# Optimization experiments

Hardware: AMD Instinct MI355X
Metric: run time of the kernel (lower is better)

Reference implementation:

```python
import jax, jax.numpy as jnp
import numpy as np

L = 104          # atom feature / hidden dim (self.length)
NUM_CLASSES = 500
D, N, P = 256, 1024, 8  # DAGs, nodes per DAG (topo-ordered), max predecessors


def setup_inputs() -> dict:
    key = jax.random.key(0)
    ks = jax.random.split(key, 8)
    atom_features = jax.random.normal(ks[0], (D, N, L), dtype=jnp.float32)

    # Padded predecessor lists; pred_idx[d, n, p] < n guarantees topological order 0..N-1.
    rng = np.random.default_rng(0)
    base = np.floor(rng.random((D, N, P)) * np.maximum(np.arange(N), 1)[None, :, None]).astype(np.int32)
    keep = rng.random((D, N, P)) < 0.6
    keep[:, :, 0] = True                      # every non-root node has >=1 predecessor
    pred_idx = np.where(keep, base, -1)
    pred_idx[:, 0, :] = -1                    # node 0 is the root (no predecessors)
    pred_idx = jnp.asarray(pred_idx, dtype=jnp.int32)

    s1 = float(1.0 / np.sqrt(L))
    s2 = float(1.0 / np.sqrt(2 * L))
    W_single = jax.random.uniform(ks[1], (L, L), minval=-s1, maxval=s1)
    b_single = jax.random.uniform(ks[2], (L,), minval=-s1, maxval=s1)
    W_merge = jax.random.uniform(ks[3], (L, 2 * L), minval=-s2, maxval=s2)
    b_merge = jax.random.uniform(ks[4], (L,), minval=-s2, maxval=s2)
    attn_w = jax.random.uniform(ks[5], (L,))   # torch.rand(length)
    dag_w = jax.random.uniform(ks[6], (L,))
    W_final = jax.random.uniform(ks[7], (NUM_CLASSES, L), minval=-s1, maxval=s1)
    b_final = jnp.zeros((NUM_CLASSES,), jnp.float32)
    return {
        "atom_features": atom_features, "pred_idx": pred_idx,
        "W_single": W_single, "b_single": b_single,
        "W_merge": W_merge, "b_merge": b_merge,
        "attn_w": attn_w, "dag_w": dag_w,
        "W_final": W_final, "b_final": b_final,
    }


def _forward(atom_features, pred_idx, W_single, b_single, W_merge, b_merge,
             attn_w, dag_w, W_final, b_final):
    n_nodes = atom_features.shape[1]

    def per_dag(feats, preds):  # feats [N, L], preds [N, P]
        def step(outputs, n):
            feat = feats[n]                                   # [L]
            p = preds[n]                                      # [P]
            valid = p >= 0                                    # [P]
            po = outputs[jnp.clip(p, 0, n_nodes - 1)]         # [P, L] gathered predecessor outputs
            # softmax over the predecessor (stacking) dim, weighted by attention_weight
            logits = jnp.where(valid[:, None], attn_w * po, -1e30)
            agg = jnp.sum(jax.nn.softmax(logits, axis=0) * po * valid[:, None].astype(po.dtype), axis=0)  # [L]
            merged = jax.nn.relu(W_merge @ jnp.concatenate([agg, feat]) + b_merge)
            root = jax.nn.relu(W_single @ feat + b_single)
            out = jnp.where(jnp.any(valid), merged, root)     # [L]
            return outputs.at[n].set(out), None
        outputs, _ = jax.lax.scan(step, jnp.zeros_like(feats), jnp.arange(n_nodes))
        return outputs[-1]                                    # output of last (sink) node

    last = jax.vmap(per_dag)(atom_features, pred_idx)         # [D, L]
    w = jax.nn.softmax(dag_w * last, axis=0)                  # softmax over DAG dim
    pooled = jnp.sum(w * last, axis=0)                        # [L]
    return pooled @ W_final.T + b_final                       # [NUM_CLASSES]


def reference(atom_features, pred_idx, W_single, b_single, W_merge, b_merge,
              attn_w, dag_w, W_final, b_final):
    return _forward(atom_features, pred_idx, W_single, b_single, W_merge, b_merge,
                    attn_w, dag_w, W_final, b_final)
```

## Files before the change

kernel.cpp:

```cpp
#include <hip/hip_runtime.h>

#define DN  256
#define NN  1024
#define PP  8
#define LL  104
#define CLS 500
#define BT  512
#define TMAX 64
#define KP  232
#define NG  26

typedef __attribute__((ext_vector_type(8))) short short8;
typedef __attribute__((ext_vector_type(4))) short short4v;
typedef __attribute__((ext_vector_type(4))) float f32x4;

#define MFMA(a, b, c) __builtin_amdgcn_mfma_f32_16x16x32_bf16((a), (b), (c), 0, 0, 0)

__device__ __forceinline__ void split_bf16(float x, unsigned short& h, unsigned short& l) {
    unsigned u = __float_as_uint(x);
    h = (unsigned short)(u >> 16);
    float hf = __uint_as_float(u & 0xFFFF0000u);
    l = (unsigned short)(__float_as_uint(x - hf) >> 16);
}

__global__ __launch_bounds__(BT, 2) void dag_level_kernel(
    const float* __restrict__ atom,
    const int*   __restrict__ pred,
    const float* __restrict__ W_single,
    const float* __restrict__ b_single,
    const float* __restrict__ W_merge,
    const float* __restrict__ b_merge,
    const float* __restrict__ attn_w,
    float* __restrict__ out_all,
    float* __restrict__ last_buf)
{
    __shared__ __align__(16) unsigned short x_hi[TMAX][KP];
    __shared__ __align__(16) unsigned short x_lo[TMAX][KP];
    __shared__ int   lvl[NN];
    __shared__ int   cnt[NN];
    __shared__ unsigned short order[NN];
    __shared__ __align__(16) float s_attn[LL];
    __shared__ float s_bm[LL];
    __shared__ int   csum[64];
    __shared__ int   s_flag, s_maxlvl;

    const int d    = blockIdx.x;
    const int tid  = threadIdx.x;
    const int wid  = tid >> 6;
    const int lane = tid & 63;
    const int p    = wid & 3;

    const float* atom_d = atom + (size_t)d * NN * LL;
    const int*   pred_d = pred + (size_t)d * NN * PP;
    float*       out_d  = out_all + (size_t)d * NN * LL;

    short8 wh[2][7], wl[2][7];
    #pragma unroll
    for (int h = 0; h < 2; ++h) {
        const int r = (2*p + h)*16 + (lane & 15);
        #pragma unroll
        for (int kt = 0; kt < 7; ++kt) {
            const int k0 = kt*32 + (lane >> 4)*8;
            short8 hh, lo8;
            #pragma unroll
            for (int j = 0; j < 8; ++j) {
                float v = (r < LL && (k0 + j) < 2*LL) ? W_merge[r*2*LL + k0 + j] : 0.f;
                unsigned short a, b;
                split_bf16(v, a, b);
                hh[j] = (short)a; lo8[j] = (short)b;
            }
            wh[h][kt] = hh; wl[h][kt] = lo8;
        }
    }

    for (int idx = tid; idx < TMAX * (KP - 2*LL); idx += BT) {
        int rr = idx / (KP - 2*LL), cc = 2*LL + (idx - rr*(KP - 2*LL));
        x_hi[rr][cc] = 0; x_lo[rr][cc] = 0;
    }
    if (tid < LL) { s_attn[tid] = attn_w[tid]; s_bm[tid] = b_merge[tid]; }
    if (tid == 0) { s_flag = 0; s_maxlvl = 0; }

    int mypA[PP], mypB[PP];
    {
        const int4* p4 = (const int4*)(pred_d + tid * PP);
        int4 a = p4[0], b = p4[1];
        mypA[0]=a.x; mypA[1]=a.y; mypA[2]=a.z; mypA[3]=a.w;
        mypA[4]=b.x; mypA[5]=b.y; mypA[6]=b.z; mypA[7]=b.w;
        const int4* q4 = (const int4*)(pred_d + (tid + BT) * PP);
        int4 c = q4[0], e = q4[1];
        mypB[0]=c.x; mypB[1]=c.y; mypB[2]=c.z; mypB[3]=c.w;
        mypB[4]=e.x; mypB[5]=e.y; mypB[6]=e.z; mypB[7]=e.w;
    }
    lvl[tid] = 0; lvl[tid + BT] = 0;
    __syncthreads();
    for (int it = 1; it <= NN; ++it) {
        int mxA = -1, mxB = -1;
        #pragma unroll
        for (int q = 0; q < PP; ++q) {
            if (mypA[q] >= 0) mxA = max(mxA, lvl[mypA[q]]);
            if (mypB[q] >= 0) mxB = max(mxB, lvl[mypB[q]]);
        }
        bool ch = false;
        if (mxA + 1 != lvl[tid])      { lvl[tid]      = mxA + 1; ch = true; }
        if (mxB + 1 != lvl[tid + BT]) { lvl[tid + BT] = mxB + 1; ch = true; }
        if (ch) s_flag = it;
        __syncthreads();
        int f = s_flag;
        __syncthreads();
        if (f != it) break;
    }
    atomicMax(&s_maxlvl, max(lvl[tid], lvl[tid + BT]));

    cnt[tid] = 0; cnt[tid + BT] = 0;
    __syncthreads();
    atomicAdd(&cnt[lvl[tid]], 1);
    atomicAdd(&cnt[lvl[tid + BT]], 1);
    __syncthreads();
    if (tid < 64) { int s = 0; for (int i = 0; i < 16; ++i) s += cnt[tid*16 + i]; csum[tid] = s; }
    __syncthreads();
    if (tid == 0) { int run = 0; for (int t = 0; t < 64; ++t) { int c = csum[t]; csum[t] = run; run += c; } }
    __syncthreads();
    if (tid < 64) {
        int run = csum[tid];
        for (int i = 0; i < 16; ++i) { int c = cnt[tid*16 + i]; cnt[tid*16 + i] = run; run += c; }
    }
    __syncthreads();
    {
        int pos = atomicAdd(&cnt[lvl[tid]], 1);      order[pos] = (unsigned short)tid;
        pos     = atomicAdd(&cnt[lvl[tid + BT]], 1); order[pos] = (unsigned short)(tid + BT);
    }
    __syncthreads();

    {
        int nroots = cnt[0];
        for (int task = tid; task < nroots * LL; task += BT) {
            int ni = task / LL, r = task - ni * LL;
            int n = order[ni];
            float acc = b_single[r];
            const float* feat = atom_d + n * LL;
            const float* wr = W_single + r * LL;
            #pragma unroll 8
            for (int l = 0; l < LL; ++l) acc = fmaf(wr[l], feat[l], acc);
            float v = fmaxf(acc, 0.f);
            out_d[n * LL + r] = v;
            if (n == NN - 1) last_buf[d * LL + r] = v;
        }
    }
    __syncthreads();

    const int maxlvl = s_maxlvl;
    for (int L = 1; L <= maxlvl; ++L) {
        const int s = cnt[L - 1], e = cnt[L];
        for (int t0 = s; t0 < e; t0 += TMAX) {
            const int tc = min(TMAX, e - t0);

            const int ntask = tc * NG;
            for (int task = tid; task < ntask; task += BT) {
                int ni = task / NG;
                int lg = task - ni * NG;
                int n  = order[t0 + ni];
                const int4* pp4 = (const int4*)(pred_d + n * PP);
                int4 pa = pp4[0], pb = pp4[1];
                int pi[PP] = {pa.x, pa.y, pa.z, pa.w, pb.x, pb.y, pb.z, pb.w};
                float4 aw = *(const float4*)&s_attn[lg*4];
                float4 ft = *(const float4*)&atom_d[n*LL + lg*4];
                float awv[4] = {aw.x, aw.y, aw.z, aw.w};
                float ftv[4] = {ft.x, ft.y, ft.z, ft.w};
                float po[PP][4];
                #pragma unroll
                for (int q = 0; q < PP; ++q) {
                    if (pi[q] >= 0) {
                        float4 t = *(const float4*)&out_d[pi[q]*LL + lg*4];
                        po[q][0] = t.x; po[q][1] = t.y; po[q][2] = t.z; po[q][3] = t.w;
                    } else {
                        po[q][0] = po[q][1] = po[q][2] = po[q][3] = 0.f;
                    }
                }
                unsigned short oh[8], ol[8];
                #pragma unroll
                for (int f = 0; f < 4; ++f) {
                    float m = -1e30f;
                    #pragma unroll
                    for (int q = 0; q < PP; ++q)
                        if (pi[q] >= 0) m = fmaxf(m, awv[f] * po[q][f]);
                    float den = 0.f, num = 0.f;
                    #pragma unroll
                    for (int q = 0; q < PP; ++q) {
                        if (pi[q] >= 0) {
                            float e2 = __expf(fmaf(awv[f], po[q][f], -m));
                            den += e2;
                            num = fmaf(e2, po[q][f], num);
                        }
                    }
                    float agg = __fdividef(num, den);
                    split_bf16(agg,    oh[f],     ol[f]);
                    split_bf16(ftv[f], oh[4 + f], ol[4 + f]);
                }
                short4v h0 = {(short)oh[0], (short)oh[1], (short)oh[2], (short)oh[3]};
                short4v l0 = {(short)ol[0], (short)ol[1], (short)ol[2], (short)ol[3]};
                short4v h1 = {(short)oh[4], (short)oh[5], (short)oh[6], (short)oh[7]};
                short4v l1 = {(short)ol[4], (short)ol[5], (short)ol[6], (short)ol[7]};
                *(short4v*)&x_hi[ni][lg*4]      = h0;
                *(short4v*)&x_lo[ni][lg*4]      = l0;
                *(short4v*)&x_hi[ni][LL + lg*4] = h1;
                *(short4v*)&x_lo[ni][LL + lg*4] = l1;
            }
            __syncthreads();

            const int mts = (tc + 15) >> 4;
            const int njobs = mts * 4;
            for (int job = wid; job < njobs; job += 8) {
                const int mt = job >> 2;
                const int row_a = mt*16 + (lane & 15);
                const int kg = (lane >> 4) * 8;
                f32x4 acc0 = {0.f,0.f,0.f,0.f}, acc1 = {0.f,0.f,0.f,0.f};
                #pragma unroll
                for (int kt = 0; kt < 7; ++kt) {
                    const int k0 = kt*32 + kg;
                    short8 ah = *(const short8*)&x_hi[row_a][k0];
                    short8 al = *(const short8*)&x_lo[row_a][k0];
                    acc0 = MFMA(ah, wh[0][kt], acc0);
                    acc0 = MFMA(ah, wl[0][kt], acc0);
                    acc0 = MFMA(al, wh[0][kt], acc0);
                    if (p < 3) {
                        acc1 = MFMA(ah, wh[1][kt], acc1);
                        acc1 = MFMA(ah, wl[1][kt], acc1);
                        acc1 = MFMA(al, wh[1][kt], acc1);
                    }
                }
                const int r0 = p*32 + (lane & 15);
                #pragma unroll
                for (int j = 0; j < 4; ++j) {
                    int ni = mt*16 + (lane >> 4)*4 + j;
                    if (ni < tc) {
                        int n = order[t0 + ni];
                        if (r0 < LL) {
                            float v = fmaxf(acc0[j] + s_bm[r0], 0.f);
                            out_d[n*LL + r0] = v;
                            if (n == NN - 1) last_buf[d*LL + r0] = v;
                        }
                        if (p < 3) {
                            const int r1 = r0 + 16;
                            float v = fmaxf(acc1[j] + s_bm[r1], 0.f);
                            out_d[n*LL + r1] = v;
                            if (n == NN - 1) last_buf[d*LL + r1] = v;
                        }
                    }
                }
            }
            __syncthreads();
        }
    }
}

__global__ __launch_bounds__(256) void final_pool_kernel(
    const float* __restrict__ last_buf,
    const float* __restrict__ dag_w,
    const float* __restrict__ W_final,
    const float* __restrict__ b_final,
    float* __restrict__ out)
{
    __shared__ float s_pooled[LL];
    const int tid = threadIdx.x;

    if (tid < LL) {
        float dw = dag_w[tid];
        float m = -1e30f;
        #pragma unroll 8
        for (int dd = 0; dd < DN; ++dd)
            m = fmaxf(m, dw * last_buf[dd * LL + tid]);
        float den = 0.f, num = 0.f;
        #pragma unroll 8
        for (int dd = 0; dd < DN; ++dd) {
            float v = last_buf[dd * LL + tid];
            float e = __expf(dw * v - m);
            den += e;
            num = fmaf(e, v, num);
        }
        s_pooled[tid] = num / den;
    }
    __syncthreads();

    for (int c = tid; c < CLS; c += 256) {
        float acc = b_final[c];
        const float* wr = W_final + c * LL;
        #pragma unroll 8
        for (int l = 0; l < LL; ++l) acc = fmaf(wr[l], s_pooled[l], acc);
        out[c] = acc;
    }
}

extern "C" void kernel_launch(void* const* d_in, const int* in_sizes, int n_in,
                              void* d_out, int out_size, void* d_ws, size_t ws_size,
                              hipStream_t stream) {
    const float* atom     = (const float*)d_in[0];
    const int*   pred     = (const int*)  d_in[1];
    const float* W_single = (const float*)d_in[2];
    const float* b_single = (const float*)d_in[3];
    const float* W_merge  = (const float*)d_in[4];
    const float* b_merge  = (const float*)d_in[5];
    const float* attn_w   = (const float*)d_in[6];
    const float* dag_w    = (const float*)d_in[7];
    const float* W_final  = (const float*)d_in[8];
    const float* b_final  = (const float*)d_in[9];
    float* out = (float*)d_out;

    float* out_all  = (float*)d_ws;
    float* last_buf = out_all + (size_t)DN * NN * LL;

    dag_level_kernel<<<DN, BT, 0, stream>>>(atom, pred, W_single, b_single,
                                            W_merge, b_merge, attn_w,
                                            out_all, last_buf);
    final_pool_kernel<<<1, 256, 0, stream>>>(last_buf, dag_w, W_final, b_final, out);
}
```

Measured before the change: 396.1 us.

## Prefetch next tile's predecessor gathers across the MFMA phase and split accumulators

```diff
diff --git a/kernel.cpp b/kernel.cpp
--- a/kernel.cpp
+++ b/kernel.cpp
@@ -80,8 +80,8 @@
     if (tid < LL) { s_attn[tid] = attn_w[tid]; s_bm[tid] = b_merge[tid]; }
     if (tid == 0) { s_flag = 0; s_maxlvl = 0; }
 
-    int mypA[PP], mypB[PP];
     {
+        int mypA[PP], mypB[PP];
         const int4* p4 = (const int4*)(pred_d + tid * PP);
         int4 a = p4[0], b = p4[1];
         mypA[0]=a.x; mypA[1]=a.y; mypA[2]=a.z; mypA[3]=a.w;
@@ -90,26 +90,26 @@
         int4 c = q4[0], e = q4[1];
         mypB[0]=c.x; mypB[1]=c.y; mypB[2]=c.z; mypB[3]=c.w;
         mypB[4]=e.x; mypB[5]=e.y; mypB[6]=e.z; mypB[7]=e.w;
-    }
-    lvl[tid] = 0; lvl[tid + BT] = 0;
-    __syncthreads();
-    for (int it = 1; it <= NN; ++it) {
-        int mxA = -1, mxB = -1;
-        #pragma unroll
-        for (int q = 0; q < PP; ++q) {
-            if (mypA[q] >= 0) mxA = max(mxA, lvl[mypA[q]]);
-            if (mypB[q] >= 0) mxB = max(mxB, lvl[mypB[q]]);
+        lvl[tid] = 0; lvl[tid + BT] = 0;
+        __syncthreads();
+        for (int it = 1; it <= NN; ++it) {
+            int mxA = -1, mxB = -1;
+            #pragma unroll
+            for (int q = 0; q < PP; ++q) {
+                if (mypA[q] >= 0) mxA = max(mxA, lvl[mypA[q]]);
+                if (mypB[q] >= 0) mxB = max(mxB, lvl[mypB[q]]);
+            }
+            bool ch = false;
+            if (mxA + 1 != lvl[tid])      { lvl[tid]      = mxA + 1; ch = true; }
+            if (mxB + 1 != lvl[tid + BT]) { lvl[tid + BT] = mxB + 1; ch = true; }
+            if (ch) s_flag = it;
+            __syncthreads();
+            int f = s_flag;
+            __syncthreads();
+            if (f != it) break;
         }
-        bool ch = false;
-        if (mxA + 1 != lvl[tid])      { lvl[tid]      = mxA + 1; ch = true; }
-        if (mxB + 1 != lvl[tid + BT]) { lvl[tid + BT] = mxB + 1; ch = true; }
-        if (ch) s_flag = it;
-        __syncthreads();
-        int f = s_flag;
-        __syncthreads();
-        if (f != it) break;
-    }
-    atomicMax(&s_maxlvl, max(lvl[tid], lvl[tid + BT]));
+        atomicMax(&s_maxlvl, max(lvl[tid], lvl[tid + BT]));
+    }
 
     cnt[tid] = 0; cnt[tid + BT] = 0;
     __syncthreads();
@@ -149,63 +149,147 @@
     __syncthreads();
 
     const int maxlvl = s_maxlvl;
+
+    int    pf_pi[PP];
+    float  pf_po[PP][4];
+    float4 pf_ft = {0.f, 0.f, 0.f, 0.f};
+    int    pf_fresh = 0;
+    bool   pf_valid = false;
+
+#define DO_PREFETCH(NT0, NTC, FIN)                                              \
+    {                                                                           \
+        pf_valid = (tid < (NTC) * NG);                                          \
+        pf_fresh = 0;                                                           \
+        if (pf_valid) {                                                         \
+            int ni_ = tid / NG, lg_ = tid - ni_ * NG;                           \
+            int n_ = order[(NT0) + ni_];                                        \
+            const int4* pp4_ = (const int4*)(pred_d + n_ * PP);                 \
+            int4 pa_ = pp4_[0], pb_ = pp4_[1];                                  \
+            pf_pi[0]=pa_.x; pf_pi[1]=pa_.y; pf_pi[2]=pa_.z; pf_pi[3]=pa_.w;     \
+            pf_pi[4]=pb_.x; pf_pi[5]=pb_.y; pf_pi[6]=pb_.z; pf_pi[7]=pb_.w;     \
+            pf_ft = *(const float4*)&atom_d[n_ * LL + lg_ * 4];                 \
+            _Pragma("unroll")                                                   \
+            for (int q_ = 0; q_ < PP; ++q_) {                                   \
+                pf_po[q_][0]=0.f; pf_po[q_][1]=0.f; pf_po[q_][2]=0.f; pf_po[q_][3]=0.f; \
+                if (pf_pi[q_] >= 0) {                                           \
+                    if (lvl[pf_pi[q_]] <= (FIN)) {                              \
+                        float4 t_ = *(const float4*)&out_d[pf_pi[q_] * LL + lg_ * 4]; \
+                        pf_po[q_][0]=t_.x; pf_po[q_][1]=t_.y; pf_po[q_][2]=t_.z; pf_po[q_][3]=t_.w; \
+                    } else pf_fresh |= (1 << q_);                               \
+                }                                                               \
+            }                                                                   \
+        }                                                                       \
+    }
+
+#define EMIT_X(NI, LG, PI, PO, FTV)                                             \
+    {                                                                           \
+        float4 aw_ = *(const float4*)&s_attn[(LG) * 4];                         \
+        float awv_[4] = {aw_.x, aw_.y, aw_.z, aw_.w};                           \
+        unsigned short oh_[8], ol_[8];                                          \
+        _Pragma("unroll")                                                       \
+        for (int f_ = 0; f_ < 4; ++f_) {                                        \
+            float m_ = -1e30f;                                                  \
+            _Pragma("unroll")                                                   \
+            for (int q_ = 0; q_ < PP; ++q_)                                     \
+                if ((PI)[q_] >= 0) m_ = fmaxf(m_, awv_[f_] * (PO)[q_][f_]);     \
+            float den_ = 0.f, num_ = 0.f;                                       \
+            _Pragma("unroll")                                                   \
+            for (int q_ = 0; q_ < PP; ++q_) {                                   \
+                if ((PI)[q_] >= 0) {                                            \
+                    float e_ = __expf(fmaf(awv_[f_], (PO)[q_][f_], -m_));       \
+                    den_ += e_;                                                 \
+                    num_ = fmaf(e_, (PO)[q_][f_], num_);                        \
+                }                                                               \
+            }                                                                   \
+            float agg_ = __fdividef(num_, den_);                                \
+            split_bf16(agg_,      oh_[f_],     ol_[f_]);                        \
+            split_bf16((FTV)[f_], oh_[4 + f_], ol_[4 + f_]);                    \
+        }                                                                       \
+        short4v h0_ = {(short)oh_[0], (short)oh_[1], (short)oh_[2], (short)oh_[3]}; \
+        short4v l0_ = {(short)ol_[0], (short)ol_[1], (short)ol_[2], (short)ol_[3]}; \
+        short4v h1_ = {(short)oh_[4], (short)oh_[5], (short)oh_[6], (short)oh_[7]}; \
+        short4v l1_ = {(short)ol_[4], (short)ol_[5], (short)ol_[6], (short)ol_[7]}; \
+        *(short4v*)&x_hi[NI][(LG)*4]      = h0_;                                \
+        *(short4v*)&x_lo[NI][(LG)*4]      = l0_;                                \
+        *(short4v*)&x_hi[NI][LL + (LG)*4] = h1_;                                \
+        *(short4v*)&x_lo[NI][LL + (LG)*4] = l1_;                                \
+    }
+
+    if (maxlvl >= 1) {
+        int ns = cnt[0], ne = cnt[1];
+        DO_PREFETCH(ns, min(TMAX, ne - ns), 0);
+    }
+
     for (int L = 1; L <= maxlvl; ++L) {
         const int s = cnt[L - 1], e = cnt[L];
         for (int t0 = s; t0 < e; t0 += TMAX) {
             const int tc = min(TMAX, e - t0);
-
             const int ntask = tc * NG;
-            for (int task = tid; task < ntask; task += BT) {
-                int ni = task / NG;
-                int lg = task - ni * NG;
-                int n  = order[t0 + ni];
+
+            const int t2 = tid + BT;
+            const bool has2 = t2 < ntask;
+            int pi2[PP]; float po2[PP][4]; float4 ft2; int ni2 = 0, lg2 = 0;
+            if (has2) {
+                ni2 = t2 / NG; lg2 = t2 - ni2 * NG;
+                int n2 = order[t0 + ni2];
+                const int4* pp4 = (const int4*)(pred_d + n2 * PP);
+                int4 pa = pp4[0], pb = pp4[1];
+                pi2[0]=pa.x; pi2[1]=pa.y; pi2[2]=pa.z; pi2[3]=pa.w;
+                pi2[4]=pb.x; pi2[5]=pb.y; pi2[6]=pb.z; pi2[7]=pb.w;
+                ft2 = *(const float4*)&atom_d[n2 * LL + lg2 * 4];
+                #pragma unroll
+                for (int q = 0; q < PP; ++q) {
+                    po2[q][0]=po2[q][1]=po2[q][2]=po2[q][3]=0.f;
+                    if (pi2[q] >= 0) {
+                        float4 t = *(const float4*)&out_d[pi2[q] * LL + lg2 * 4];
+                        po2[q][0]=t.x; po2[q][1]=t.y; po2[q][2]=t.z; po2[q][3]=t.w;
+                    }
+                }
+            }
+            if (pf_valid) {
+                int ni = tid / NG, lg = tid - ni * NG;
+                #pragma unroll
+                for (int q = 0; q < PP; ++q) {
+                    if (pf_fresh & (1 << q)) {
+                        float4 t = *(const float4*)&out_d[pf_pi[q] * LL + lg * 4];
+                        pf_po[q][0]=t.x; pf_po[q][1]=t.y; pf_po[q][2]=t.z; pf_po[q][3]=t.w;
+                    }
+                }
+                float ftv[4] = {pf_ft.x, pf_ft.y, pf_ft.z, pf_ft.w};
+                EMIT_X(ni, lg, pf_pi, pf_po, ftv);
+            }
+            if (has2) {
+                float ftv[4] = {ft2.x, ft2.y, ft2.z, ft2.w};
+                EMIT_X(ni2, lg2, pi2, po2, ftv);
+            }
+            for (int task = tid + 2*BT; task < ntask; task += BT) {
+                int ni = task / NG, lg = task - ni * NG;
+                int n = order[t0 + ni];
                 const int4* pp4 = (const int4*)(pred_d + n * PP);
                 int4 pa = pp4[0], pb = pp4[1];
                 int pi[PP] = {pa.x, pa.y, pa.z, pa.w, pb.x, pb.y, pb.z, pb.w};
-                float4 aw = *(const float4*)&s_attn[lg*4];
-                float4 ft = *(const float4*)&atom_d[n*LL + lg*4];
-                float awv[4] = {aw.x, aw.y, aw.z, aw.w};
-                float ftv[4] = {ft.x, ft.y, ft.z, ft.w};
                 float po[PP][4];
                 #pragma unroll
                 for (int q = 0; q < PP; ++q) {
+                    po[q][0]=po[q][1]=po[q][2]=po[q][3]=0.f;
                     if (pi[q] >= 0) {
-                        float4 t = *(const float4*)&out_d[pi[q]*LL + lg*4];
-                        po[q][0] = t.x; po[q][1] = t.y; po[q][2] = t.z; po[q][3] = t.w;
-                    } else {
-                        po[q][0] = po[q][1] = po[q][2] = po[q][3] = 0.f;
+                        float4 t = *(const float4*)&out_d[pi[q] * LL + lg * 4];
+                        po[q][0]=t.x; po[q][1]=t.y; po[q][2]=t.z; po[q][3]=t.w;
                     }
                 }
-                unsigned short oh[8], ol[8];
-                #pragma unroll
-                for (int f = 0; f < 4; ++f) {
-                    float m = -1e30f;
-                    #pragma unroll
-                    for (int q = 0; q < PP; ++q)
-                        if (pi[q] >= 0) m = fmaxf(m, awv[f] * po[q][f]);
-                    float den = 0.f, num = 0.f;
-                    #pragma unroll
-                    for (int q = 0; q < PP; ++q) {
-                        if (pi[q] >= 0) {
-                            float e2 = __expf(fmaf(awv[f], po[q][f], -m));
-                            den += e2;
-                            num = fmaf(e2, po[q][f], num);
-                        }
-                    }
-                    float agg = __fdividef(num, den);
-                    split_bf16(agg,    oh[f],     ol[f]);
-                    split_bf16(ftv[f], oh[4 + f], ol[4 + f]);
-                }
-                short4v h0 = {(short)oh[0], (short)oh[1], (short)oh[2], (short)oh[3]};
-                short4v l0 = {(short)ol[0], (short)ol[1], (short)ol[2], (short)ol[3]};
-                short4v h1 = {(short)oh[4], (short)oh[5], (short)oh[6], (short)oh[7]};
-                short4v l1 = {(short)ol[4], (short)ol[5], (short)ol[6], (short)ol[7]};
-                *(short4v*)&x_hi[ni][lg*4]      = h0;
-                *(short4v*)&x_lo[ni][lg*4]      = l0;
-                *(short4v*)&x_hi[ni][LL + lg*4] = h1;
-                *(short4v*)&x_lo[ni][LL + lg*4] = l1;
+                float4 ft = *(const float4*)&atom_d[n * LL + lg * 4];
+                float ftv[4] = {ft.x, ft.y, ft.z, ft.w};
+                EMIT_X(ni, lg, pi, po, ftv);
             }
             __syncthreads();
+
+            {
+                int nt0 = -1, ntc = 0;
+                if (t0 + TMAX < e)           { nt0 = t0 + TMAX; ntc = min(TMAX, e - nt0); }
+                else if (L + 1 <= maxlvl)    { nt0 = e;         ntc = min(TMAX, cnt[L + 1] - e); }
+                if (ntc > 0) { DO_PREFETCH(nt0, ntc, L - 1); }
+                else pf_valid = false;
+            }
 
             const int mts = (tc + 15) >> 4;
             const int njobs = mts * 4;
@@ -213,21 +297,24 @@
                 const int mt = job >> 2;
                 const int row_a = mt*16 + (lane & 15);
                 const int kg = (lane >> 4) * 8;
-                f32x4 acc0 = {0.f,0.f,0.f,0.f}, acc1 = {0.f,0.f,0.f,0.f};
+                f32x4 a0 = {0.f,0.f,0.f,0.f}, b0 = {0.f,0.f,0.f,0.f}, c0 = {0.f,0.f,0.f,0.f};
+                f32x4 a1 = {0.f,0.f,0.f,0.f}, b1 = {0.f,0.f,0.f,0.f}, c1 = {0.f,0.f,0.f,0.f};
                 #pragma unroll
                 for (int kt = 0; kt < 7; ++kt) {
                     const int k0 = kt*32 + kg;
                     short8 ah = *(const short8*)&x_hi[row_a][k0];
                     short8 al = *(const short8*)&x_lo[row_a][k0];
-                    acc0 = MFMA(ah, wh[0][kt], acc0);
-                    acc0 = MFMA(ah, wl[0][kt], acc0);
-                    acc0 = MFMA(al, wh[0][kt], acc0);
+                    a0 = MFMA(ah, wh[0][kt], a0);
+                    b0 = MFMA(ah, wl[0][kt], b0);
+                    c0 = MFMA(al, wh[0][kt], c0);
                     if (p < 3) {
-                        acc1 = MFMA(ah, wh[1][kt], acc1);
-                        acc1 = MFMA(ah, wl[1][kt], acc1);
-                        acc1 = MFMA(al, wh[1][kt], acc1);
+                        a1 = MFMA(ah, wh[1][kt], a1);
+                        b1 = MFMA(ah, wl[1][kt], b1);
+                        c1 = MFMA(al, wh[1][kt], c1);
                     }
                 }
+                f32x4 acc0 = a0 + b0 + c0;
+                f32x4 acc1 = a1 + b1 + c1;
                 const int r0 = p*32 + (lane & 15);
                 #pragma unroll
                 for (int j = 0; j < 4; ++j) {
```

Result: slower. 641.1 us (+61.8%).
